# Optimization experiments

Measured on AMD Instinct MI355X. Metric: run time of the kernel, lower is better.

## Reference

```python
import jax, jax.numpy as jnp
import numpy as np

B, V, NQ, D, HEADS, FF, NL = 2, 8, 336, 256, 8, 1024, 6
H_IMG, W_IMG = 512, 512


def setup_inputs() -> dict:
    key = jax.random.key(0)
    ks = iter(jax.random.split(key, 48))
    def n(shape, s=0.02):
        return jax.random.normal(next(ks), shape, dtype=jnp.float32) * s
    inp = {}
    inp["tgt"] = jnp.zeros((B, NQ, D), jnp.float32)
    inp["query_pos"] = jax.random.normal(next(ks), (B, NQ, D), jnp.float32)
    inp["reference_points"] = jax.random.uniform(next(ks), (B, NQ, 3), dtype=jnp.float32)
    inp["feat0"] = jax.random.normal(next(ks), (B, V, D, 64, 64), jnp.float32)
    inp["feat1"] = jax.random.normal(next(ks), (B, V, D, 32, 32), jnp.float32)
    inp["feat2"] = jax.random.normal(next(ks), (B, V, D, 16, 16), jnp.float32)
    # cameras: near-identity rotations, translation pushed +2 in z so points project in front
    inp["camera_R"] = jnp.broadcast_to(jnp.eye(3, dtype=jnp.float32), (B, V, 3, 3)) + n((B, V, 3, 3), 0.1)
    T = n((B, V, 3), 0.1)
    inp["camera_T"] = T.at[..., 2].add(2.0)
    K = jnp.array([[500.0, 0.0, 256.0], [0.0, 500.0, 256.0], [0.0, 0.0, 1.0]], jnp.float32)
    inp["camera_K"] = jnp.broadcast_to(K, (B, V, 3, 3))
    # decoder params (stacked over NL layers)
    inp["Wqkv"] = n((NL, 3 * D, D)); inp["bqkv"] = jnp.zeros((NL, 3 * D), jnp.float32)
    inp["Wo"] = n((NL, D, D));       inp["bo"] = jnp.zeros((NL, D), jnp.float32)
    inp["ln1_g"] = jnp.ones((NL, D), jnp.float32); inp["ln1_b"] = jnp.zeros((NL, D), jnp.float32)
    inp["Wproj"] = n((NL, D, D));    inp["bproj"] = jnp.zeros((NL, D), jnp.float32)
    inp["pn_g"] = jnp.ones((NL, D), jnp.float32); inp["pn_b"] = jnp.zeros((NL, D), jnp.float32)
    inp["W1"] = n((NL, FF, D));      inp["b1"] = jnp.zeros((NL, FF), jnp.float32)
    inp["W2"] = n((NL, D, FF));      inp["b2"] = jnp.zeros((NL, D), jnp.float32)
    inp["ln2_g"] = jnp.ones((NL, D), jnp.float32); inp["ln2_b"] = jnp.zeros((NL, D), jnp.float32)
    inp["pose_W0"] = n((D, D)); inp["pose_b0"] = jnp.zeros((D,), jnp.float32)
    inp["pose_W1"] = n((D, D)); inp["pose_b1"] = jnp.zeros((D,), jnp.float32)
    inp["pose_W2"] = n((3, D)); inp["pose_b2"] = jnp.zeros((3,), jnp.float32)
    inp["cls_W"] = n((1, D));   inp["cls_b"] = jnp.zeros((1,), jnp.float32)
    return inp


def _layer_norm(x, g, b):
    m = x.mean(-1, keepdims=True)
    v = ((x - m) ** 2).mean(-1, keepdims=True)
    return (x - m) * jax.lax.rsqrt(v + 1e-5) * g + b


def _project(pts, R, T, K):
    # pts (B,NQ,3) -> cam coords per view: pts @ R^T + T
    p = jnp.einsum('bqc,bvdc->bvqd', pts, R) + T[:, :, None, :]  # (B,V,NQ,3)
    z = jnp.clip(p[..., 2], 0.1, None)
    fx = K[..., 0, 0][:, :, None]; fy = K[..., 1, 1][:, :, None]
    cx = K[..., 0, 2][:, :, None]; cy = K[..., 1, 2][:, :, None]
    u = p[..., 0] * fx / z + cx
    v = p[..., 1] * fy / z + cy
    un = 2.0 * u / (W_IMG - 1) - 1.0
    vn = 2.0 * v / (H_IMG - 1) - 1.0
    mask = (un > -1.0) & (un < 1.0) & (vn > -1.0) & (vn < 1.0) & (p[..., 2] > 0)
    return jnp.stack([un, vn], -1), mask  # (B,V,NQ,2), (B,V,NQ)


def _sample(feats, grid):
    # bilinear point sampling == F.grid_sample(align_corners=False, padding_mode='zeros')
    C, Hh, Ww = feats.shape[2], feats.shape[3], feats.shape[4]
    f = feats.reshape(B * V, C, Hh, Ww)
    g = grid.reshape(B * V, NQ, 2)
    x = (g[..., 0] + 1.0) * Ww * 0.5 - 0.5
    y = (g[..., 1] + 1.0) * Hh * 0.5 - 0.5
    x0f = jnp.floor(x); y0f = jnp.floor(y)
    ix0 = x0f.astype(jnp.int32); iy0 = y0f.astype(jnp.int32)
    ix1 = ix0 + 1; iy1 = iy0 + 1
    wx1 = (x - x0f)[:, None, :]; wx0 = 1.0 - wx1
    wy1 = (y - y0f)[:, None, :]; wy0 = 1.0 - wy1
    def gat(ix, iy):
        valid = ((ix >= 0) & (ix < Ww) & (iy >= 0) & (iy < Hh)).astype(f.dtype)[:, None, :]
        ixc = jnp.clip(ix, 0, Ww - 1); iyc = jnp.clip(iy, 0, Hh - 1)
        vals = jax.vmap(lambda ff, yy, xx: ff[:, yy, xx])(f, iyc, ixc)  # (BV,C,NQ)
        return vals * valid
    out = (gat(ix0, iy0) * wy0 * wx0 + gat(ix1, iy0) * wy0 * wx1 +
           gat(ix0, iy1) * wy1 * wx0 + gat(ix1, iy1) * wy1 * wx1)
    return out.reshape(B, V, C, NQ).transpose(0, 1, 3, 2)  # (B,V,NQ,C)


def _mha(xq, xv, Wqkv, bqkv, Wo, bo):
    hd = D // HEADS
    q = (xq @ Wqkv[:D].T + bqkv[:D]).reshape(B, NQ, HEADS, hd)
    k = (xq @ Wqkv[D:2 * D].T + bqkv[D:2 * D]).reshape(B, NQ, HEADS, hd)
    v = (xv @ Wqkv[2 * D:].T + bqkv[2 * D:]).reshape(B, NQ, HEADS, hd)
    att = jax.nn.softmax(jnp.einsum('bqhd,bkhd->bhqk', q, k) * (1.0 / np.sqrt(hd)), axis=-1)
    o = jnp.einsum('bhqk,bkhd->bqhd', att, v).reshape(B, NQ, D)
    return o @ Wo.T + bo


def reference(tgt, query_pos, reference_points, feat0, feat1, feat2, camera_R, camera_T, camera_K,
              Wqkv, bqkv, Wo, bo, ln1_g, ln1_b, Wproj, bproj, pn_g, pn_b,
              W1, b1, W2, b2, ln2_g, ln2_b,
              pose_W0, pose_b0, pose_W1, pose_b1, pose_W2, pose_b2, cls_W, cls_b):
    out = tgt
    ref = reference_points
    feats = (feat0, feat1, feat2)
    logits_all, poses_all = [], []
    for l in range(NL):
        # self-attention (dropout = eval identity)
        qk = out + query_pos
        out = _layer_norm(out + _mha(qk, out, Wqkv[l], bqkv[l], Wo[l], bo[l]), ln1_g[l], ln1_b[l])
        # projective attention: project 3D refs, grid-sample all levels, mask-fuse across views
        grid, mask = _project(ref, camera_R, camera_T, camera_K)
        ms = (_sample(feats[0], grid) + _sample(feats[1], grid) + _sample(feats[2], grid)) / 3.0
        vm = mask[..., None].astype(out.dtype)  # (B,V,NQ,1)
        fused = (ms * vm).sum(1) / jnp.clip(vm.sum(1), 1.0, None)  # (B,NQ,D)
        out = _layer_norm(out + fused @ Wproj[l].T + bproj[l], pn_g[l], pn_b[l])
        # FFN
        ffn = jax.nn.relu(out @ W1[l].T + b1[l]) @ W2[l].T + b2[l]
        out = _layer_norm(out + ffn, ln2_g[l], ln2_b[l])
        # iterative pose refinement + classification head
        h = jax.nn.relu(out @ pose_W0.T + pose_b0)
        h = jax.nn.relu(h @ pose_W1.T + pose_b1)
        ref = ref + h @ pose_W2.T + pose_b2
        logits_all.append(out @ cls_W.T + cls_b)
        poses_all.append(ref)
    # (NL,B,NQ,1) logits ++ (NL,B,NQ,3) poses -> (NL,B,NQ,4)
    return jnp.concatenate([jnp.stack(logits_all), jnp.stack(poses_all)], axis=-1)
```

## Files before the change

kernel.cpp:

```cpp
#include <hip/hip_runtime.h>
#include <math.h>

#define BB 2
#define VV 8
#define NQ 336
#define DD 256
#define HEADS 8
#define HD 32
#define FF 1024
#define NL 6
#define BQ (BB*NQ)
#define W_IMG 512
#define H_IMG 512
#define MROWS BQ

__device__ __forceinline__ void job_transpose2(float* tile, int b,
                                               const float* __restrict__ f0,
                                               const float* __restrict__ f1,
                                               const float* __restrict__ f2,
                                               float* __restrict__ o0,
                                               float* __restrict__ o1,
                                               float* __restrict__ o2) {
    const float* src; float* dst; int HW, ptiles;
    if (b < 2048)      { src = f0; dst = o0; HW = 4096; ptiles = 64; }
    else if (b < 2560) { b -= 2048; src = f1; dst = o1; HW = 1024; ptiles = 16; }
    else               { b -= 2560; src = f2; dst = o2; HW = 256;  ptiles = 4;  }
    int cg = b & 1;
    int pt = (b >> 1) % ptiles;
    int bv = (b >> 1) / ptiles;
    int d0 = cg * 128, p0 = pt * 64;
    int t = threadIdx.x;
    int t4 = t >> 4, t15 = t & 15;
    #pragma unroll
    for (int pass = 0; pass < 8; ++pass) {
        int d = pass * 16 + t4;
        int p = t15 * 4;
        float4 v = *(const float4*)(src + ((size_t)(bv * DD + d0 + d)) * HW + p0 + p);
        tile[d * 65 + p + 0] = v.x; tile[d * 65 + p + 1] = v.y;
        tile[d * 65 + p + 2] = v.z; tile[d * 65 + p + 3] = v.w;
    }
    __syncthreads();
    int c4 = (t & 31) * 4, pxb = t >> 5;
    #pragma unroll
    for (int pass = 0; pass < 8; ++pass) {
        int px = pass * 8 + pxb;
        float4 o;
        o.x = tile[(c4 + 0) * 65 + px];
        o.y = tile[(c4 + 1) * 65 + px];
        o.z = tile[(c4 + 2) * 65 + px];
        o.w = tile[(c4 + 3) * 65 + px];
        *(float4*)(dst + ((size_t)bv * HW + p0 + px) * DD + d0 + c4) = o;
    }
}

__global__ __launch_bounds__(256) void init_k(const float* __restrict__ tgt,
                                              const float* __restrict__ qp,
                                              const float* __restrict__ refpts,
                                              float* __restrict__ x,
                                              float* __restrict__ xq,
                                              float* __restrict__ refb) {
    int i = blockIdx.x * 256 + threadIdx.x;
    float4 tv = ((const float4*)tgt)[i];
    float4 qv = ((const float4*)qp)[i];
    ((float4*)x)[i] = tv;
    ((float4*)xq)[i] = make_float4(tv.x + qv.x, tv.y + qv.y, tv.z + qv.z, tv.w + qv.w);
    if (i < BQ * 3) refb[i] = refpts[i];
}

__device__ __forceinline__ void job_qkv(float* sm, int bid,
                                        const float* __restrict__ Aq,
                                        const float* __restrict__ Ax,
                                        const float* __restrict__ W,
                                        const float* __restrict__ bias,
                                        float* __restrict__ Qp,
                                        float* __restrict__ Kp,
                                        float* __restrict__ Vp) {
    float* At = sm;
    float* Wt = sm + 1088;
    int t = threadIdx.x;
    int m0 = (bid % 21) * 32;
    int ncol = bid / 21;
    int n0 = ncol * 64;
    const float* A = (ncol < 8) ? Aq : Ax;
    int tx = t & 15, ty = t >> 4;
    int nc = n0 + tx * 4;
    float acc0[4], acc1[4];
    {
        float4 bv = *(const float4*)(bias + nc);
        acc0[0] = bv.x; acc0[1] = bv.y; acc0[2] = bv.z; acc0[3] = bv.w;
        acc1[0] = bv.x; acc1[1] = bv.y; acc1[2] = bv.z; acc1[3] = bv.w;
    }
    int am = t >> 3, ak4 = (t & 7) * 4;
    for (int kt = 0; kt < 8; ++kt) {
        int kk = kt * 32;
        __syncthreads();
        {
            float4 v = *(const float4*)(A + (size_t)(m0 + am) * DD + kk + ak4);
            At[(ak4 + 0) * 34 + am] = v.x; At[(ak4 + 1) * 34 + am] = v.y;
            At[(ak4 + 2) * 34 + am] = v.z; At[(ak4 + 3) * 34 + am] = v.w;
        }
        #pragma unroll
        for (int s = 0; s < 2; ++s) {
            int idx = t + s * 256;
            int wn = idx >> 3, wk4 = (idx & 7) * 4;
            float4 v = *(const float4*)(W + (size_t)(n0 + wn) * DD + kk + wk4);
            Wt[(wk4 + 0) * 68 + wn] = v.x; Wt[(wk4 + 1) * 68 + wn] = v.y;
            Wt[(wk4 + 2) * 68 + wn] = v.z; Wt[(wk4 + 3) * 68 + wn] = v.w;
        }
        __syncthreads();
        #pragma unroll
        for (int k = 0; k < 32; ++k) {
            float2 av = *(const float2*)&At[k * 34 + ty * 2];
            float4 wv = *(const float4*)&Wt[k * 68 + tx * 4];
            acc0[0] = fmaf(av.x, wv.x, acc0[0]); acc0[1] = fmaf(av.x, wv.y, acc0[1]);
            acc0[2] = fmaf(av.x, wv.z, acc0[2]); acc0[3] = fmaf(av.x, wv.w, acc0[3]);
            acc1[0] = fmaf(av.y, wv.x, acc1[0]); acc1[1] = fmaf(av.y, wv.y, acc1[1]);
            acc1[2] = fmaf(av.y, wv.z, acc1[2]); acc1[3] = fmaf(av.y, wv.w, acc1[3]);
        }
    }
    int mr = m0 + ty * 2;
    int kind = nc >> 8;
    float* base = kind == 0 ? Qp : (kind == 1 ? Kp : Vp);
    int h = (nc >> 5) & 7, d4 = nc & 31;
    #pragma unroll
    for (int i = 0; i < 2; ++i) {
        int m = mr + i;
        int b = m / NQ, q = m - b * NQ;
        float* p = base + ((size_t)((b << 3) + h) * NQ + q) * HD + d4;
        float* src = i == 0 ? acc0 : acc1;
        *(float4*)p = make_float4(src[0], src[1], src[2], src[3]);
    }
}

__device__ __forceinline__ void job_pose(float* sm, int job,
                                         const float* __restrict__ x,
                                         const float* __restrict__ W0, const float* __restrict__ b0,
                                         const float* __restrict__ W1p, const float* __restrict__ b1p,
                                         const float* __restrict__ W2p, const float* __restrict__ b2p,
                                         const float* __restrict__ cW, const float* __restrict__ cb,
                                         float* __restrict__ refb, float* __restrict__ outp) {
    float* sX  = sm;
    float* sH  = sm + 1024;
    float* red = sm + 2048;
    int r0 = job * 4;
    int tid = threadIdx.x;
    ((float4*)sX)[tid] = ((const float4*)(x + (size_t)r0 * DD))[tid];
    __syncthreads();
    {
        float a0 = b0[tid], a1 = a0, a2 = a0, a3 = a0;
        const float* wp = W0 + (size_t)tid * DD;
        for (int k = 0; k < DD; k += 4) {
            float4 w  = *(const float4*)(wp + k);
            float4 x0 = *(const float4*)(sX + 0 * DD + k);
            float4 x1 = *(const float4*)(sX + 1 * DD + k);
            float4 x2 = *(const float4*)(sX + 2 * DD + k);
            float4 x3 = *(const float4*)(sX + 3 * DD + k);
            a0 = fmaf(x0.x, w.x, a0); a0 = fmaf(x0.y, w.y, a0); a0 = fmaf(x0.z, w.z, a0); a0 = fmaf(x0.w, w.w, a0);
            a1 = fmaf(x1.x, w.x, a1); a1 = fmaf(x1.y, w.y, a1); a1 = fmaf(x1.z, w.z, a1); a1 = fmaf(x1.w, w.w, a1);
            a2 = fmaf(x2.x, w.x, a2); a2 = fmaf(x2.y, w.y, a2); a2 = fmaf(x2.z, w.z, a2); a2 = fmaf(x2.w, w.w, a2);
            a3 = fmaf(x3.x, w.x, a3); a3 = fmaf(x3.y, w.y, a3); a3 = fmaf(x3.z, w.z, a3); a3 = fmaf(x3.w, w.w, a3);
        }
        sH[0 * DD + tid] = fmaxf(a0, 0.f);
        sH[1 * DD + tid] = fmaxf(a1, 0.f);
        sH[2 * DD + tid] = fmaxf(a2, 0.f);
        sH[3 * DD + tid] = fmaxf(a3, 0.f);
    }
    __syncthreads();
    float h[4];
    {
        float a0 = b1p[tid], a1 = a0, a2 = a0, a3 = a0;
        const float* wp = W1p + (size_t)tid * DD;
        for (int k = 0; k < DD; k += 4) {
            float4 w  = *(const float4*)(wp + k);
            float4 x0 = *(const float4*)(sH + 0 * DD + k);
            float4 x1 = *(const float4*)(sH + 1 * DD + k);
            float4 x2 = *(const float4*)(sH + 2 * DD + k);
            float4 x3 = *(const float4*)(sH + 3 * DD + k);
            a0 = fmaf(x0.x, w.x, a0); a0 = fmaf(x0.y, w.y, a0); a0 = fmaf(x0.z, w.z, a0); a0 = fmaf(x0.w, w.w, a0);
            a1 = fmaf(x1.x, w.x, a1); a1 = fmaf(x1.y, w.y, a1); a1 = fmaf(x1.z, w.z, a1); a1 = fmaf(x1.w, w.w, a1);
            a2 = fmaf(x2.x, w.x, a2); a2 = fmaf(x2.y, w.y, a2); a2 = fmaf(x2.z, w.z, a2); a2 = fmaf(x2.w, w.w, a2);
            a3 = fmaf(x3.x, w.x, a3); a3 = fmaf(x3.y, w.y, a3); a3 = fmaf(x3.z, w.z, a3); a3 = fmaf(x3.w, w.w, a3);
        }
        h[0] = fmaxf(a0, 0.f); h[1] = fmaxf(a1, 0.f); h[2] = fmaxf(a2, 0.f); h[3] = fmaxf(a3, 0.f);
    }
    float w2a = W2p[tid], w2b = W2p[DD + tid], w2c = W2p[2 * DD + tid], cw = cW[tid];
    float v[4][4];
    #pragma unroll
    for (int r = 0; r < 4; ++r) {
        v[r][0] = h[r] * w2a;
        v[r][1] = h[r] * w2b;
        v[r][2] = h[r] * w2c;
        v[r][3] = sX[r * DD + tid] * cw;
    }
    #pragma unroll
    for (int o2 = 32; o2 > 0; o2 >>= 1) {
        #pragma unroll
        for (int r = 0; r < 4; ++r) {
            #pragma unroll
            for (int c = 0; c < 4; ++c) v[r][c] += __shfl_xor(v[r][c], o2);
        }
    }
    int wid = tid >> 6, lane = tid & 63;
    if (lane == 0) {
        #pragma unroll
        for (int r = 0; r < 4; ++r) {
            #pragma unroll
            for (int c = 0; c < 4; ++c) red[(r * 4 + c) * 4 + wid] = v[r][c];
        }
    }
    __syncthreads();
    if (tid < 4) {
        int r = tid;
        float d0 = red[(r * 4 + 0) * 4 + 0] + red[(r * 4 + 0) * 4 + 1] + red[(r * 4 + 0) * 4 + 2] + red[(r * 4 + 0) * 4 + 3] + b2p[0];
        float d1 = red[(r * 4 + 1) * 4 + 0] + red[(r * 4 + 1) * 4 + 1] + red[(r * 4 + 1) * 4 + 2] + red[(r * 4 + 1) * 4 + 3] + b2p[1];
        float d2 = red[(r * 4 + 2) * 4 + 0] + red[(r * 4 + 2) * 4 + 1] + red[(r * 4 + 2) * 4 + 2] + red[(r * 4 + 2) * 4 + 3] + b2p[2];
        float cl = red[(r * 4 + 3) * 4 + 0] + red[(r * 4 + 3) * 4 + 1] + red[(r * 4 + 3) * 4 + 2] + red[(r * 4 + 3) * 4 + 3] + cb[0];
        int row = r0 + r;
        float rx = refb[(size_t)row * 3 + 0] + d0;
        float ry = refb[(size_t)row * 3 + 1] + d1;
        float rz = refb[(size_t)row * 3 + 2] + d2;
        refb[(size_t)row * 3 + 0] = rx;
        refb[(size_t)row * 3 + 1] = ry;
        refb[(size_t)row * 3 + 2] = rz;
        outp[(size_t)row * 4 + 0] = cl;
        outp[(size_t)row * 4 + 1] = rx;
        outp[(size_t)row * 4 + 2] = ry;
        outp[(size_t)row * 4 + 3] = rz;
    }
}

__global__ __launch_bounds__(256) void qkv_pose(const float* __restrict__ xq,
                                                const float* __restrict__ x,
                                                const float* __restrict__ Wqkv,
                                                const float* __restrict__ bqkv,
                                                float* __restrict__ Qp,
                                                float* __restrict__ Kp,
                                                float* __restrict__ Vp,
                                                const float* __restrict__ pW0, const float* __restrict__ pb0,
                                                const float* __restrict__ pW1, const float* __restrict__ pb1,
                                                const float* __restrict__ pW2, const float* __restrict__ pb2,
                                                const float* __restrict__ cW, const float* __restrict__ cb,
                                                float* __restrict__ refb, float* __restrict__ outp) {
    __shared__ float sm[3264];
    if (blockIdx.x < 252)
        job_qkv(sm, blockIdx.x, xq, x, Wqkv, bqkv, Qp, Kp, Vp);
    else
        job_pose(sm, blockIdx.x - 252, x, pW0, pb0, pW1, pb1, pW2, pb2, cW, cb, refb, outp);
}

__global__ __launch_bounds__(256) void qkv_tr(const float* __restrict__ xq,
                                              const float* __restrict__ x,
                                              const float* __restrict__ Wqkv,
                                              const float* __restrict__ bqkv,
                                              float* __restrict__ Qp,
                                              float* __restrict__ Kp,
                                              float* __restrict__ Vp,
                                              const float* __restrict__ f0,
                                              const float* __restrict__ f1,
                                              const float* __restrict__ f2,
                                              float* __restrict__ o0,
                                              float* __restrict__ o1,
                                              float* __restrict__ o2) {
    __shared__ float sm[8320];
    if (blockIdx.x < 252)
        job_qkv(sm, blockIdx.x, xq, x, Wqkv, bqkv, Qp, Kp, Vp);
    else
        job_transpose2(sm, blockIdx.x - 252, f0, f1, f2, o0, o1, o2);
}

__global__ __launch_bounds__(256) void pose_only(const float* __restrict__ x,
                                                 const float* __restrict__ pW0, const float* __restrict__ pb0,
                                                 const float* __restrict__ pW1, const float* __restrict__ pb1,
                                                 const float* __restrict__ pW2, const float* __restrict__ pb2,
                                                 const float* __restrict__ cW, const float* __restrict__ cb,
                                                 float* __restrict__ refb, float* __restrict__ outp) {
    __shared__ float sm[2112];
    job_pose(sm, blockIdx.x, x, pW0, pb0, pW1, pb1, pW2, pb2, cW, cb, refb, outp);
}

__global__ __launch_bounds__(256) void attn_fused(const float* __restrict__ Qp,
                                                  const float* __restrict__ Kp,
                                                  const float* __restrict__ Vp,
                                                  float* __restrict__ O,
                                                  const float* __restrict__ f0,
                                                  const float* __restrict__ f1,
                                                  const float* __restrict__ f2,
                                                  float* __restrict__ o0,
                                                  float* __restrict__ o1,
                                                  float* __restrict__ o2) {
    extern __shared__ float sm[];
    int blk = blockIdx.x;
    if (blk >= 176) { job_transpose2(sm, blk - 176 + 1344, f0, f1, f2, o0, o1, o2); return; }
    float* S   = sm;
    float* KT  = sm + 11008;
    float* U   = sm + 13184;
    float* inv = sm + 15232;
    int bh = blk & 15, qt = blk >> 4;
    int t = threadIdx.x;
    const float scale = 0.17677669529663687f;
    const float* Qb = Qp + (size_t)bh * NQ * HD;
    const float* Kb = Kp + (size_t)bh * NQ * HD;
    const float* Vb = Vp + (size_t)bh * NQ * HD;
    {
        int ql = t >> 3, d4 = (t & 7) * 4;
        int qg = qt * 32 + ql;
        float4 v = (qg < NQ) ? *(const float4*)(Qb + (size_t)qg * HD + d4)
                             : make_float4(0.f, 0.f, 0.f, 0.f);
        U[(d4 + 0) * 36 + ql] = v.x * scale;
        U[(d4 + 1) * 36 + ql] = v.y * scale;
        U[(d4 + 2) * 36 + ql] = v.z * scale;
        U[(d4 + 3) * 36 + ql] = v.w * scale;
    }
    int tx = t & 15, ty = t >> 4;
    for (int kt = 0; kt < 6; ++kt) {
        __syncthreads();
        #pragma unroll
        for (int s = 0; s < 2; ++s) {
            int idx = t + s * 256;
            int kl = idx >> 3, d4 = (idx & 7) * 4;
            int kg = kt * 64 + kl;
            float4 v = (kg < NQ) ? *(const float4*)(Kb + (size_t)kg * HD + d4)
                                 : make_float4(0.f, 0.f, 0.f, 0.f);
            KT[(d4 + 0) * 68 + kl] = v.x; KT[(d4 + 1) * 68 + kl] = v.y;
            KT[(d4 + 2) * 68 + kl] = v.z; KT[(d4 + 3) * 68 + kl] = v.w;
        }
        __syncthreads();
        float a0[4] = {0, 0, 0, 0}, a1[4] = {0, 0, 0, 0};
        #pragma unroll
        for (int k = 0; k < 32; ++k) {
            float2 qv = *(const float2*)&U[k * 36 + ty * 2];
            float4 kv = *(const float4*)&KT[k * 68 + tx * 4];
            a0[0] = fmaf(qv.x, kv.x, a0[0]); a0[1] = fmaf(qv.x, kv.y, a0[1]);
            a0[2] = fmaf(qv.x, kv.z, a0[2]); a0[3] = fmaf(qv.x, kv.w, a0[3]);
            a1[0] = fmaf(qv.y, kv.x, a1[0]); a1[1] = fmaf(qv.y, kv.y, a1[1]);
            a1[2] = fmaf(qv.y, kv.z, a1[2]); a1[3] = fmaf(qv.y, kv.w, a1[3]);
        }
        int col = kt * 64 + tx * 4;
        if (col < NQ) {
            *(float4*)&S[(ty * 2 + 0) * 344 + col] = make_float4(a0[0], a0[1], a0[2], a0[3]);
            *(float4*)&S[(ty * 2 + 1) * 344 + col] = make_float4(a1[0], a1[1], a1[2], a1[3]);
        }
    }
    __syncthreads();
    {
        int r = t >> 3, cg = t & 7;
        float* row = S + (size_t)r * 344;
        float m = -1e30f;
        for (int i = 0; i < 42; ++i) m = fmaxf(m, row[cg + 8 * i]);
        m = fmaxf(m, __shfl_xor(m, 1));
        m = fmaxf(m, __shfl_xor(m, 2));
        m = fmaxf(m, __shfl_xor(m, 4));
        float ssum = 0.f;
        for (int i = 0; i < 42; ++i) {
            float e = expf(row[cg + 8 * i] - m);
            row[cg + 8 * i] = e;
            ssum += e;
        }
        ssum += __shfl_xor(ssum, 1);
        ssum += __shfl_xor(ssum, 2);
        ssum += __shfl_xor(ssum, 4);
        if (cg == 0) inv[r] = 1.f / ssum;
    }
    int q = t >> 3, d0 = (t & 7) * 4;
    float acc[4] = {0, 0, 0, 0};
    for (int kt = 0; kt < 6; ++kt) {
        __syncthreads();
        #pragma unroll
        for (int s = 0; s < 2; ++s) {
            int idx = t + s * 256;
            int kl = idx >> 3, d4 = (idx & 7) * 4;
            int kg = kt * 64 + kl;
            float4 v = (kg < NQ) ? *(const float4*)(Vb + (size_t)kg * HD + d4)
                                 : make_float4(0.f, 0.f, 0.f, 0.f);
            *(float4*)&U[kl * 32 + d4] = v;
        }
        __syncthreads();
        int kmax = (kt == 5) ? 16 : 64;
        const float* Srow = S + (size_t)q * 344 + kt * 64;
        #pragma unroll 8
        for (int kk = 0; kk < kmax; ++kk) {
            float p = Srow[kk];
            float4 vv = *(const float4*)&U[kk * 32 + d0];
            acc[0] = fmaf(p, vv.x, acc[0]); acc[1] = fmaf(p, vv.y, acc[1]);
            acc[2] = fmaf(p, vv.z, acc[2]); acc[3] = fmaf(p, vv.w, acc[3]);
        }
    }
    float iv = inv[q];
    int qg = qt * 32 + q;
    int b = bh >> 3, h = bh & 7;
    if (qg < NQ)
        *(float4*)(O + ((size_t)(b * NQ + qg)) * DD + h * HD + d0) =
            make_float4(acc[0] * iv, acc[1] * iv, acc[2] * iv, acc[3] * iv);
}

__device__ __forceinline__ void job_gemm_ln(float* sm, int r0,
                                            const float* __restrict__ A,
                                            const float* __restrict__ Wt,
                                            const float* __restrict__ bias,
                                            const float* __restrict__ gam,
                                            const float* __restrict__ bet,
                                            float* __restrict__ x) {
    float* sA    = sm;
    float* redS  = sm + 1024;
    float* redS2 = sm + 1040;
    float* mu    = sm + 1056;
    float* ri    = sm + 1060;
    int j = threadIdx.x;
    ((float4*)sA)[j] = ((const float4*)(A + (size_t)r0 * DD))[j];
    __syncthreads();
    float acc0 = bias[j], acc1 = acc0, acc2 = acc0, acc3 = acc0;
    const float* wp = Wt + (size_t)j * DD;
    for (int k = 0; k < DD; k += 4) {
        float4 w  = *(const float4*)(wp + k);
        float4 a0 = *(const float4*)(sA + 0 * DD + k);
        float4 a1 = *(const float4*)(sA + 1 * DD + k);
        float4 a2 = *(const float4*)(sA + 2 * DD + k);
        float4 a3 = *(const float4*)(sA + 3 * DD + k);
        acc0 = fmaf(a0.x, w.x, acc0); acc0 = fmaf(a0.y, w.y, acc0); acc0 = fmaf(a0.z, w.z, acc0); acc0 = fmaf(a0.w, w.w, acc0);
        acc1 = fmaf(a1.x, w.x, acc1); acc1 = fmaf(a1.y, w.y, acc1); acc1 = fmaf(a1.z, w.z, acc1); acc1 = fmaf(a1.w, w.w, acc1);
        acc2 = fmaf(a2.x, w.x, acc2); acc2 = fmaf(a2.y, w.y, acc2); acc2 = fmaf(a2.z, w.z, acc2); acc2 = fmaf(a2.w, w.w, acc2);
        acc3 = fmaf(a3.x, w.x, acc3); acc3 = fmaf(a3.y, w.y, acc3); acc3 = fmaf(a3.z, w.z, acc3); acc3 = fmaf(a3.w, w.w, acc3);
    }
    float val[4];
    val[0] = x[(size_t)(r0 + 0) * DD + j] + acc0;
    val[1] = x[(size_t)(r0 + 1) * DD + j] + acc1;
    val[2] = x[(size_t)(r0 + 2) * DD + j] + acc2;
    val[3] = x[(size_t)(r0 + 3) * DD + j] + acc3;
    float s[4], s2[4];
    #pragma unroll
    for (int r = 0; r < 4; ++r) { s[r] = val[r]; s2[r] = val[r] * val[r]; }
    #pragma unroll
    for (int o2 = 32; o2 > 0; o2 >>= 1) {
        #pragma unroll
        for (int r = 0; r < 4; ++r) {
            s[r]  += __shfl_xor(s[r],  o2);
            s2[r] += __shfl_xor(s2[r], o2);
        }
    }
    int wid = j >> 6, lane = j & 63;
    if (lane == 0) {
        #pragma unroll
        for (int r = 0; r < 4; ++r) { redS[r * 4 + wid] = s[r]; redS2[r * 4 + wid] = s2[r]; }
    }
    __syncthreads();
    if (j < 4) {
        int r = j;
        float ts  = redS[r * 4 + 0]  + redS[r * 4 + 1]  + redS[r * 4 + 2]  + redS[r * 4 + 3];
        float ts2 = redS2[r * 4 + 0] + redS2[r * 4 + 1] + redS2[r * 4 + 2] + redS2[r * 4 + 3];
        float mean = ts * (1.f / DD);
        float var = ts2 * (1.f / DD) - mean * mean;
        mu[r] = mean;
        ri[r] = rsqrtf(var + 1e-5f);
    }
    __syncthreads();
    float g = gam[j], be = bet[j];
    #pragma unroll
    for (int r = 0; r < 4; ++r)
        x[(size_t)(r0 + r) * DD + j] = (val[r] - mu[r]) * ri[r] * g + be;
}

template <bool TRANSPOSED>
__device__ __forceinline__ void job_sample(float* sm, int row,
                                           const float* __restrict__ f0,
                                           const float* __restrict__ f1,
                                           const float* __restrict__ f2,
                                           const float* __restrict__ refb,
                                           const float* __restrict__ Rm,
                                           const float* __restrict__ Tm,
                                           const float* __restrict__ Km,
                                           float* __restrict__ fused) {
    float* sg    = sm;
    float* sPart = sm + 32;
    int t = threadIdx.x;
    int b = row / NQ;
    if (t < 8) {
        int bv = b * VV + t;
        const float* r = refb + (size_t)row * 3;
        const float* R = Rm + (size_t)bv * 9;
        const float* T = Tm + (size_t)bv * 3;
        const float* K = Km + (size_t)bv * 9;
        float p0 = R[0] * r[0] + R[1] * r[1] + R[2] * r[2] + T[0];
        float p1 = R[3] * r[0] + R[4] * r[1] + R[5] * r[2] + T[1];
        float p2 = R[6] * r[0] + R[7] * r[1] + R[8] * r[2] + T[2];
        float z = fmaxf(p2, 0.1f);
        float u  = p0 * K[0] / z + K[2];
        float vv = p1 * K[4] / z + K[5];
        float un = 2.f * u  / (float)(W_IMG - 1) - 1.f;
        float vn = 2.f * vv / (float)(H_IMG - 1) - 1.f;
        bool m = (un > -1.f) && (un < 1.f) && (vn > -1.f) && (vn < 1.f) && (p2 > 0.f);
        sg[t * 3 + 0] = un; sg[t * 3 + 1] = vn; sg[t * 3 + 2] = m ? 1.f : 0.f;
    }
    __syncthreads();
    int v = t >> 5, cg = t & 31;
    int ch0 = cg * 8;
    float acc[8] = {0, 0, 0, 0, 0, 0, 0, 0};
    float m = sg[v * 3 + 2];
    if (m != 0.f) {
        float un = sg[v * 3 + 0], vn = sg[v * 3 + 1];
        int bv = b * VV + v;
        const float* fl[3] = { f0, f1, f2 };
        const int Hs[3] = { 64, 32, 16 };
        #pragma unroll
        for (int lev = 0; lev < 3; ++lev) {
            int Hh = Hs[lev], Ww = Hs[lev];
            const float* f = fl[lev];
            float xx = (un + 1.f) * Ww * 0.5f - 0.5f;
            float yy = (vn + 1.f) * Hh * 0.5f - 0.5f;
            float x0f = floorf(xx), y0f = floorf(yy);
            int ix0 = (int)x0f, iy0 = (int)y0f;
            float wx1 = xx - x0f, wx0 = 1.f - wx1;
            float wy1 = yy - y0f, wy0 = 1.f - wy1;
            #pragma unroll
            for (int tap = 0; tap < 4; ++tap) {
                int ix = ix0 + (tap & 1);
                int iy = iy0 + (tap >> 1);
                float wgt = ((tap & 1) ? wx1 : wx0) * ((tap >> 1) ? wy1 : wy0);
                if (ix >= 0 && ix < Ww && iy >= 0 && iy < Hh) {
                    if (TRANSPOSED) {
                        const float* p = f + ((size_t)bv * Hh * Ww + (size_t)iy * Ww + ix) * DD + ch0;
                        float4 va = *(const float4*)p;
                        float4 vb = *(const float4*)(p + 4);
                        acc[0] = fmaf(wgt, va.x, acc[0]); acc[1] = fmaf(wgt, va.y, acc[1]);
                        acc[2] = fmaf(wgt, va.z, acc[2]); acc[3] = fmaf(wgt, va.w, acc[3]);
                        acc[4] = fmaf(wgt, vb.x, acc[4]); acc[5] = fmaf(wgt, vb.y, acc[5]);
                        acc[6] = fmaf(wgt, vb.z, acc[6]); acc[7] = fmaf(wgt, vb.w, acc[7]);
                    } else {
                        #pragma unroll
                        for (int c = 0; c < 8; ++c) {
                            float vv2 = f[(((size_t)bv * DD + ch0 + c) * Hh + iy) * Ww + ix];
                            acc[c] = fmaf(wgt, vv2, acc[c]);
                        }
                    }
                }
            }
        }
    }
    #pragma unroll
    for (int c = 0; c < 8; ++c) sPart[v * 258 + ch0 + c] = acc[c] * (1.f / 3.f);
    __syncthreads();
    float cnt = sg[2] + sg[5] + sg[8] + sg[11] + sg[14] + sg[17] + sg[20] + sg[23];
    float s = 0.f;
    #pragma unroll
    for (int v2 = 0; v2 < 8; ++v2) s += sPart[v2 * 258 + t];
    fused[(size_t)row * DD + t] = s / fmaxf(cnt, 1.f);
}

template <bool TRANSPOSED>
__global__ __launch_bounds__(256) void oproj_sample(const float* __restrict__ attn_o,
                                                    const float* __restrict__ Wo,
                                                    const float* __restrict__ bo,
                                                    const float* __restrict__ gam,
                                                    const float* __restrict__ bet,
                                                    float* __restrict__ x,
                                                    const float* __restrict__ f0,
                                                    const float* __restrict__ f1,
                                                    const float* __restrict__ f2,
                                                    const float* __restrict__ refb,
                                                    const float* __restrict__ Rm,
                                                    const float* __restrict__ Tm,
                                                    const float* __restrict__ Km,
                                                    float* __restrict__ fused) {
    __shared__ float sm[2112];
    if (blockIdx.x < 168)
        job_gemm_ln(sm, blockIdx.x * 4, attn_o, Wo, bo, gam, bet, x);
    else
        job_sample<TRANSPOSED>(sm, blockIdx.x - 168, f0, f1, f2, refb, Rm, Tm, Km, fused);
}

__global__ __launch_bounds__(256) void gemm4_res_ln(const float* __restrict__ A,
                                                    const float* __restrict__ Wt,
                                                    const float* __restrict__ bias,
                                                    const float* __restrict__ gam,
                                                    const float* __restrict__ bet,
                                                    float* __restrict__ x) {
    __shared__ float sm[1064];
    job_gemm_ln(sm, blockIdx.x * 4, A, Wt, bias, gam, bet, x);
}

template <int MODE>
__global__ __launch_bounds__(256) void gemm_tile(const float* __restrict__ A,
                                                 const float* __restrict__ W,
                                                 const float* __restrict__ bias,
                                                 float* __restrict__ C,
                                                 int Ktot, int Kper, int Nout) {
    __shared__ float At[32][34];
    __shared__ float Wt[32][68];
    int t = threadIdx.x;
    int m0 = blockIdx.x * 32;
    int n0 = blockIdx.y * 64;
    int kz = blockIdx.z;
    int kofs = kz * Kper;
    int tx = t & 15, ty = t >> 4;
    int nc = n0 + tx * 4;
    float acc0[4], acc1[4];
    {
        float4 bv = make_float4(0.f, 0.f, 0.f, 0.f);
        if (bias && kz == 0) bv = *(const float4*)(bias + nc);
        acc0[0] = bv.x; acc0[1] = bv.y; acc0[2] = bv.z; acc0[3] = bv.w;
        acc1[0] = bv.x; acc1[1] = bv.y; acc1[2] = bv.z; acc1[3] = bv.w;
    }
    int am = t >> 3, ak4 = (t & 7) * 4;
    int ktiles = Kper >> 5;
    for (int kt = 0; kt < ktiles; ++kt) {
        int kk = kofs + kt * 32;
        __syncthreads();
        {
            float4 v = *(const float4*)(A + (size_t)(m0 + am) * Ktot + kk + ak4);
            At[ak4 + 0][am] = v.x; At[ak4 + 1][am] = v.y;
            At[ak4 + 2][am] = v.z; At[ak4 + 3][am] = v.w;
        }
        #pragma unroll
        for (int s = 0; s < 2; ++s) {
            int idx = t + s * 256;
            int wn = idx >> 3, wk4 = (idx & 7) * 4;
            float4 v = *(const float4*)(W + (size_t)(n0 + wn) * Ktot + kk + wk4);
            Wt[wk4 + 0][wn] = v.x; Wt[wk4 + 1][wn] = v.y;
            Wt[wk4 + 2][wn] = v.z; Wt[wk4 + 3][wn] = v.w;
        }
        __syncthreads();
        #pragma unroll
        for (int k = 0; k < 32; ++k) {
            float2 av = *(const float2*)&At[k][ty * 2];
            float4 wv = *(const float4*)&Wt[k][tx * 4];
            acc0[0] = fmaf(av.x, wv.x, acc0[0]); acc0[1] = fmaf(av.x, wv.y, acc0[1]);
            acc0[2] = fmaf(av.x, wv.z, acc0[2]); acc0[3] = fmaf(av.x, wv.w, acc0[3]);
            acc1[0] = fmaf(av.y, wv.x, acc1[0]); acc1[1] = fmaf(av.y, wv.y, acc1[1]);
            acc1[2] = fmaf(av.y, wv.z, acc1[2]); acc1[3] = fmaf(av.y, wv.w, acc1[3]);
        }
    }
    if (MODE == 1) {
        #pragma unroll
        for (int j = 0; j < 4; ++j) { acc0[j] = fmaxf(acc0[j], 0.f); acc1[j] = fmaxf(acc1[j], 0.f); }
    }
    int mr = m0 + ty * 2;
    float* Cb = C + (size_t)kz * MROWS * Nout;
    *(float4*)(Cb + (size_t)mr * Nout + nc)       = make_float4(acc0[0], acc0[1], acc0[2], acc0[3]);
    *(float4*)(Cb + (size_t)(mr + 1) * Nout + nc) = make_float4(acc1[0], acc1[1], acc1[2], acc1[3]);
}

template <int NP>
__global__ __launch_bounds__(256) void ln_res(float* __restrict__ x,
                                              const float* __restrict__ C,
                                              const float* __restrict__ gam,
                                              const float* __restrict__ bet,
                                              const float* __restrict__ qp,
                                              float* __restrict__ xq) {
    __shared__ float redS[4][4], redS2[4][4];
    __shared__ float mu[4], ri[4];
    int r0 = blockIdx.x * 4;
    int j = threadIdx.x;
    float val[4];
    #pragma unroll
    for (int r = 0; r < 4; ++r) {
        float a = x[(size_t)(r0 + r) * DD + j];
        #pragma unroll
        for (int p = 0; p < NP; ++p) a += C[(size_t)p * MROWS * DD + (size_t)(r0 + r) * DD + j];
        val[r] = a;
    }
    float s[4], s2[4];
    #pragma unroll
    for (int r = 0; r < 4; ++r) { s[r] = val[r]; s2[r] = val[r] * val[r]; }
    #pragma unroll
    for (int o = 32; o > 0; o >>= 1) {
        #pragma unroll
        for (int r = 0; r < 4; ++r) {
            s[r]  += __shfl_xor(s[r],  o);
            s2[r] += __shfl_xor(s2[r], o);
        }
    }
    int wid = j >> 6, lane = j & 63;
    if (lane == 0) {
        #pragma unroll
        for (int r = 0; r < 4; ++r) { redS[r][wid] = s[r]; redS2[r][wid] = s2[r]; }
    }
    __syncthreads();
    if (j < 4) {
        int r = j;
        float ts  = redS[r][0]  + redS[r][1]  + redS[r][2]  + redS[r][3];
        float ts2 = redS2[r][0] + redS2[r][1] + redS2[r][2] + redS2[r][3];
        float mean = ts * (1.f / DD);
        float var = ts2 * (1.f / DD) - mean * mean;
        mu[r] = mean;
        ri[r] = rsqrtf(var + 1e-5f);
    }
    __syncthreads();
    float g = gam[j], be = bet[j];
    #pragma unroll
    for (int r = 0; r < 4; ++r) {
        float o = (val[r] - mu[r]) * ri[r] * g + be;
        x[(size_t)(r0 + r) * DD + j] = o;
        if (qp) xq[(size_t)(r0 + r) * DD + j] = o + qp[(size_t)(r0 + r) * DD + j];
    }
}

extern "C" void kernel_launch(void* const* d_in, const int* in_sizes, int n_in,
                              void* d_out, int out_size, void* d_ws, size_t ws_size,
                              hipStream_t stream) {
    const float* tgt       = (const float*)d_in[0];
    const float* query_pos = (const float*)d_in[1];
    const float* refpts    = (const float*)d_in[2];
    const float* feat0     = (const float*)d_in[3];
    const float* feat1     = (const float*)d_in[4];
    const float* feat2     = (const float*)d_in[5];
    const float* camR      = (const float*)d_in[6];
    const float* camT      = (const float*)d_in[7];
    const float* camK      = (const float*)d_in[8];
    const float* Wqkv      = (const float*)d_in[9];
    const float* bqkv      = (const float*)d_in[10];
    const float* Wo        = (const float*)d_in[11];
    const float* bo        = (const float*)d_in[12];
    const float* ln1_g     = (const float*)d_in[13];
    const float* ln1_b     = (const float*)d_in[14];
    const float* Wproj     = (const float*)d_in[15];
    const float* bproj     = (const float*)d_in[16];
    const float* pn_g      = (const float*)d_in[17];
    const float* pn_b      = (const float*)d_in[18];
    const float* W1        = (const float*)d_in[19];
    const float* b1        = (const float*)d_in[20];
    const float* W2        = (const float*)d_in[21];
    const float* b2        = (const float*)d_in[22];
    const float* ln2_g     = (const float*)d_in[23];
    const float* ln2_b     = (const float*)d_in[24];
    const float* pose_W0   = (const float*)d_in[25];
    const float* pose_b0   = (const float*)d_in[26];
    const float* pose_W1   = (const float*)d_in[27];
    const float* pose_b1   = (const float*)d_in[28];
    const float* pose_W2   = (const float*)d_in[29];
    const float* pose_b2   = (const float*)d_in[30];
    const float* cls_W     = (const float*)d_in[31];
    const float* cls_b     = (const float*)d_in[32];
    float* out = (float*)d_out;

    float* w = (float*)d_ws;
    size_t off = 0;
    auto alloc = [&](size_t n) { float* p = w + off; off += n; return p; };
    float* x      = alloc((size_t)BQ * DD);
    float* xq     = alloc((size_t)BQ * DD);
    float* Qp     = alloc((size_t)BB * HEADS * NQ * HD);
    float* Kp     = alloc((size_t)BB * HEADS * NQ * HD);
    float* Vp     = alloc((size_t)BB * HEADS * NQ * HD);
    float* attn_o = alloc((size_t)BQ * DD);
    float* fused  = alloc((size_t)BQ * DD);
    float* ffh    = alloc((size_t)BQ * FF);
    float* ctmp   = alloc((size_t)4 * BQ * DD);
    float* refb   = alloc((size_t)BQ * 3 + 64);
    size_t base_floats = off;
    size_t featT_floats = (size_t)BB * VV * DD * (64 * 64 + 32 * 32 + 16 * 16);
    bool useT = ws_size >= (base_floats + featT_floats) * sizeof(float);
    float *fT0 = nullptr, *fT1 = nullptr, *fT2 = nullptr;
    if (useT) {
        fT0 = alloc((size_t)BB * VV * 64 * 64 * DD);
        fT1 = alloc((size_t)BB * VV * 32 * 32 * DD);
        fT2 = alloc((size_t)BB * VV * 16 * 16 * DD);
    }

    init_k<<<168, 256, 0, stream>>>(tgt, query_pos, refpts, x, xq, refb);

    for (int l = 0; l < NL; ++l) {
        if (l == 0 && useT) {
            qkv_tr<<<252 + 1344, 256, 0, stream>>>(
                xq, x, Wqkv, bqkv, Qp, Kp, Vp,
                feat0, feat1, feat2, fT0, fT1, fT2);
        } else {
            qkv_pose<<<252 + (l > 0 ? 168 : 0), 256, 0, stream>>>(
                xq, x, Wqkv + (size_t)l * 3 * DD * DD, bqkv + (size_t)l * 3 * DD, Qp, Kp, Vp,
                pose_W0, pose_b0, pose_W1, pose_b1, pose_W2, pose_b2, cls_W, cls_b,
                refb, out + (size_t)(l - 1) * BQ * 4);
        }
        {
            int tc = (l == 0 && useT) ? 1344 : 0;
            attn_fused<<<176 + tc, 256, 61056, stream>>>(
                Qp, Kp, Vp, attn_o, feat0, feat1, feat2, fT0, fT1, fT2);
        }
        if (useT)
            oproj_sample<true><<<840, 256, 0, stream>>>(
                attn_o, Wo + (size_t)l * DD * DD, bo + (size_t)l * DD,
                ln1_g + (size_t)l * DD, ln1_b + (size_t)l * DD, x,
                fT0, fT1, fT2, refb, camR, camT, camK, fused);
        else
            oproj_sample<false><<<840, 256, 0, stream>>>(
                attn_o, Wo + (size_t)l * DD * DD, bo + (size_t)l * DD,
                ln1_g + (size_t)l * DD, ln1_b + (size_t)l * DD, x,
                feat0, feat1, feat2, refb, camR, camT, camK, fused);
        gemm4_res_ln<<<BQ / 4, 256, 0, stream>>>(
            fused, Wproj + (size_t)l * DD * DD, bproj + (size_t)l * DD,
            pn_g + (size_t)l * DD, pn_b + (size_t)l * DD, x);
        gemm_tile<1><<<dim3(21, 16, 1), 256, 0, stream>>>(
            x, W1 + (size_t)l * FF * DD, b1 + (size_t)l * FF, ffh, DD, DD, FF);
        gemm_tile<0><<<dim3(21, 4, 4), 256, 0, stream>>>(
            ffh, W2 + (size_t)l * DD * FF, b2 + (size_t)l * DD, ctmp, FF, FF / 4, DD);
        ln_res<4><<<BQ / 4, 256, 0, stream>>>(
            x, ctmp, ln2_g + (size_t)l * DD, ln2_b + (size_t)l * DD, query_pos, xq);
    }
    pose_only<<<BQ / 4, 256, 0, stream>>>(
        x, pose_W0, pose_b0, pose_W1, pose_b1, pose_W2, pose_b2, cls_W, cls_b,
        refb, out + (size_t)(NL - 1) * BQ * 4);
}
```

Measured before the change: 888.3 us.

## Fuse FFN down-projection with residual layernorm; move feature transposes out of attention

Replaces the split-K tiled FFN2 GEMM and the separate residual-LayerNorm kernel with one kernel, ffn2_ln. It handles 4 rows per block, stages the hidden activations in shared memory and has each thread compute one output column over the full K=1024. This removes the partial-sum buffer round trip and one launch per layer. The cost is per-thread strided reads of W2 rows, with every block re-reading the whole weight matrix. The feature-map transpose now uses 32-pixel tiles with twice as many blocks, and all of it runs inside the layer-0 QKV launch rather than being split with the attention kernel. The attention kernel now uses static shared memory and no longer carries transpose work.

After: 1.037 ms. 16.8% more time.

```diff
diff --git a/kernel.cpp b/kernel.cpp
--- a/kernel.cpp
+++ b/kernel.cpp
@@ -14,7 +14,7 @@
 #define H_IMG 512
 #define MROWS BQ
 
-__device__ __forceinline__ void job_transpose2(float* tile, int b,
+__device__ __forceinline__ void job_transpose3(float* tile, int b,
                                                const float* __restrict__ f0,
                                                const float* __restrict__ f1,
                                                const float* __restrict__ f2,
@@ -22,33 +22,32 @@
                                                float* __restrict__ o1,
                                                float* __restrict__ o2) {
     const float* src; float* dst; int HW, ptiles;
-    if (b < 2048)      { src = f0; dst = o0; HW = 4096; ptiles = 64; }
-    else if (b < 2560) { b -= 2048; src = f1; dst = o1; HW = 1024; ptiles = 16; }
-    else               { b -= 2560; src = f2; dst = o2; HW = 256;  ptiles = 4;  }
+    if (b < 4096)      { src = f0; dst = o0; HW = 4096; ptiles = 128; }
+    else if (b < 5120) { b -= 4096; src = f1; dst = o1; HW = 1024; ptiles = 32; }
+    else               { b -= 5120; src = f2; dst = o2; HW = 256;  ptiles = 8;  }
     int cg = b & 1;
     int pt = (b >> 1) % ptiles;
     int bv = (b >> 1) / ptiles;
-    int d0 = cg * 128, p0 = pt * 64;
+    int d0 = cg * 128, p0 = pt * 32;
     int t = threadIdx.x;
-    int t4 = t >> 4, t15 = t & 15;
-    #pragma unroll
-    for (int pass = 0; pass < 8; ++pass) {
-        int d = pass * 16 + t4;
-        int p = t15 * 4;
-        float4 v = *(const float4*)(src + ((size_t)(bv * DD + d0 + d)) * HW + p0 + p);
-        tile[d * 65 + p + 0] = v.x; tile[d * 65 + p + 1] = v.y;
-        tile[d * 65 + p + 2] = v.z; tile[d * 65 + p + 3] = v.w;
+    int chb = t >> 3, px4 = (t & 7) * 4;
+    #pragma unroll
+    for (int pass = 0; pass < 4; ++pass) {
+        int ch = pass * 32 + chb;
+        float4 v = *(const float4*)(src + ((size_t)(bv * DD + d0 + ch)) * HW + p0 + px4);
+        tile[ch * 33 + px4 + 0] = v.x; tile[ch * 33 + px4 + 1] = v.y;
+        tile[ch * 33 + px4 + 2] = v.z; tile[ch * 33 + px4 + 3] = v.w;
     }
     __syncthreads();
     int c4 = (t & 31) * 4, pxb = t >> 5;
     #pragma unroll
-    for (int pass = 0; pass < 8; ++pass) {
+    for (int pass = 0; pass < 4; ++pass) {
         int px = pass * 8 + pxb;
         float4 o;
-        o.x = tile[(c4 + 0) * 65 + px];
-        o.y = tile[(c4 + 1) * 65 + px];
-        o.z = tile[(c4 + 2) * 65 + px];
-        o.w = tile[(c4 + 3) * 65 + px];
+        o.x = tile[(c4 + 0) * 33 + px];
+        o.y = tile[(c4 + 1) * 33 + px];
+        o.z = tile[(c4 + 2) * 33 + px];
+        o.w = tile[(c4 + 3) * 33 + px];
         *(float4*)(dst + ((size_t)bv * HW + p0 + px) * DD + d0 + c4) = o;
     }
 }
@@ -261,11 +260,11 @@
                                               float* __restrict__ o0,
                                               float* __restrict__ o1,
                                               float* __restrict__ o2) {
-    __shared__ float sm[8320];
+    __shared__ float sm[4224];
     if (blockIdx.x < 252)
         job_qkv(sm, blockIdx.x, xq, x, Wqkv, bqkv, Qp, Kp, Vp);
     else
-        job_transpose2(sm, blockIdx.x - 252, f0, f1, f2, o0, o1, o2);
+        job_transpose3(sm, blockIdx.x - 252, f0, f1, f2, o0, o1, o2);
 }
 
 __global__ __launch_bounds__(256) void pose_only(const float* __restrict__ x,
@@ -281,20 +280,13 @@
 __global__ __launch_bounds__(256) void attn_fused(const float* __restrict__ Qp,
                                                   const float* __restrict__ Kp,
                                                   const float* __restrict__ Vp,
-                                                  float* __restrict__ O,
-                                                  const float* __restrict__ f0,
-                                                  const float* __restrict__ f1,
-                                                  const float* __restrict__ f2,
-                                                  float* __restrict__ o0,
-                                                  float* __restrict__ o1,
-                                                  float* __restrict__ o2) {
-    extern __shared__ float sm[];
-    int blk = blockIdx.x;
-    if (blk >= 176) { job_transpose2(sm, blk - 176 + 1344, f0, f1, f2, o0, o1, o2); return; }
+                                                  float* __restrict__ O) {
+    __shared__ float sm[15264];
     float* S   = sm;
     float* KT  = sm + 11008;
     float* U   = sm + 13184;
     float* inv = sm + 15232;
+    int blk = blockIdx.x;
     int bh = blk & 15, qt = blk >> 4;
     int t = threadIdx.x;
     const float scale = 0.17677669529663687f;
@@ -457,6 +449,76 @@
     #pragma unroll
     for (int r = 0; r < 4; ++r)
         x[(size_t)(r0 + r) * DD + j] = (val[r] - mu[r]) * ri[r] * g + be;
+}
+
+__global__ __launch_bounds__(256) void ffn2_ln(const float* __restrict__ ffh,
+                                               const float* __restrict__ W2,
+                                               const float* __restrict__ b2,
+                                               const float* __restrict__ gam,
+                                               const float* __restrict__ bet,
+                                               float* __restrict__ x,
+                                               const float* __restrict__ qp,
+                                               float* __restrict__ xq) {
+    __shared__ float sH[4 * FF];
+    __shared__ float redS[16], redS2[16], mu[4], ri[4];
+    int r0 = blockIdx.x * 4;
+    int j = threadIdx.x;
+    #pragma unroll
+    for (int s = 0; s < 4; ++s)
+        ((float4*)sH)[j + s * 256] = ((const float4*)(ffh + (size_t)r0 * FF))[j + s * 256];
+    __syncthreads();
+    float acc0 = b2[j], acc1 = acc0, acc2 = acc0, acc3 = acc0;
+    const float* wp = W2 + (size_t)j * FF;
+    for (int k = 0; k < FF; k += 4) {
+        float4 w  = *(const float4*)(wp + k);
+        float4 a0 = *(const float4*)(sH + 0 * FF + k);
+        float4 a1 = *(const float4*)(sH + 1 * FF + k);
+        float4 a2 = *(const float4*)(sH + 2 * FF + k);
+        float4 a3 = *(const float4*)(sH + 3 * FF + k);
+        acc0 = fmaf(a0.x, w.x, acc0); acc0 = fmaf(a0.y, w.y, acc0); acc0 = fmaf(a0.z, w.z, acc0); acc0 = fmaf(a0.w, w.w, acc0);
+        acc1 = fmaf(a1.x, w.x, acc1); acc1 = fmaf(a1.y, w.y, acc1); acc1 = fmaf(a1.z, w.z, acc1); acc1 = fmaf(a1.w, w.w, acc1);
+        acc2 = fmaf(a2.x, w.x, acc2); acc2 = fmaf(a2.y, w.y, acc2); acc2 = fmaf(a2.z, w.z, acc2); acc2 = fmaf(a2.w, w.w, acc2);
+        acc3 = fmaf(a3.x, w.x, acc3); acc3 = fmaf(a3.y, w.y, acc3); acc3 = fmaf(a3.z, w.z, acc3); acc3 = fmaf(a3.w, w.w, acc3);
+    }
+    float val[4];
+    val[0] = x[(size_t)(r0 + 0) * DD + j] + acc0;
+    val[1] = x[(size_t)(r0 + 1) * DD + j] + acc1;
+    val[2] = x[(size_t)(r0 + 2) * DD + j] + acc2;
+    val[3] = x[(size_t)(r0 + 3) * DD + j] + acc3;
+    float s[4], s2[4];
+    #pragma unroll
+    for (int r = 0; r < 4; ++r) { s[r] = val[r]; s2[r] = val[r] * val[r]; }
+    #pragma unroll
+    for (int o2 = 32; o2 > 0; o2 >>= 1) {
+        #pragma unroll
+        for (int r = 0; r < 4; ++r) {
+            s[r]  += __shfl_xor(s[r],  o2);
+            s2[r] += __shfl_xor(s2[r], o2);
+        }
+    }
+    int wid = j >> 6, lane = j & 63;
+    if (lane == 0) {
+        #pragma unroll
+        for (int r = 0; r < 4; ++r) { redS[r * 4 + wid] = s[r]; redS2[r * 4 + wid] = s2[r]; }
+    }
+    __syncthreads();
+    if (j < 4) {
+        int r = j;
+        float ts  = redS[r * 4 + 0]  + redS[r * 4 + 1]  + redS[r * 4 + 2]  + redS[r * 4 + 3];
+        float ts2 = redS2[r * 4 + 0] + redS2[r * 4 + 1] + redS2[r * 4 + 2] + redS2[r * 4 + 3];
+        float mean = ts * (1.f / DD);
+        float var = ts2 * (1.f / DD) - mean * mean;
+        mu[r] = mean;
+        ri[r] = rsqrtf(var + 1e-5f);
+    }
+    __syncthreads();
+    float g = gam[j], be = bet[j];
+    #pragma unroll
+    for (int r = 0; r < 4; ++r) {
+        float o = (val[r] - mu[r]) * ri[r] * g + be;
+        x[(size_t)(r0 + r) * DD + j] = o;
+        xq[(size_t)(r0 + r) * DD + j] = o + qp[(size_t)(r0 + r) * DD + j];
+    }
 }
 
 template <bool TRANSPOSED>
@@ -636,61 +698,6 @@
     float* Cb = C + (size_t)kz * MROWS * Nout;
     *(float4*)(Cb + (size_t)mr * Nout + nc)       = make_float4(acc0[0], acc0[1], acc0[2], acc0[3]);
     *(float4*)(Cb + (size_t)(mr + 1) * Nout + nc) = make_float4(acc1[0], acc1[1], acc1[2], acc1[3]);
-}
-
-template <int NP>
-__global__ __launch_bounds__(256) void ln_res(float* __restrict__ x,
-                                              const float* __restrict__ C,
-                                              const float* __restrict__ gam,
-                                              const float* __restrict__ bet,
-                                              const float* __restrict__ qp,
-                                              float* __restrict__ xq) {
-    __shared__ float redS[4][4], redS2[4][4];
-    __shared__ float mu[4], ri[4];
-    int r0 = blockIdx.x * 4;
-    int j = threadIdx.x;
-    float val[4];
-    #pragma unroll
-    for (int r = 0; r < 4; ++r) {
-        float a = x[(size_t)(r0 + r) * DD + j];
-        #pragma unroll
-        for (int p = 0; p < NP; ++p) a += C[(size_t)p * MROWS * DD + (size_t)(r0 + r) * DD + j];
-        val[r] = a;
-    }
-    float s[4], s2[4];
-    #pragma unroll
-    for (int r = 0; r < 4; ++r) { s[r] = val[r]; s2[r] = val[r] * val[r]; }
-    #pragma unroll
-    for (int o = 32; o > 0; o >>= 1) {
-        #pragma unroll
-        for (int r = 0; r < 4; ++r) {
-            s[r]  += __shfl_xor(s[r],  o);
-            s2[r] += __shfl_xor(s2[r], o);
-        }
-    }
-    int wid = j >> 6, lane = j & 63;
-    if (lane == 0) {
-        #pragma unroll
-        for (int r = 0; r < 4; ++r) { redS[r][wid] = s[r]; redS2[r][wid] = s2[r]; }
-    }
-    __syncthreads();
-    if (j < 4) {
-        int r = j;
-        float ts  = redS[r][0]  + redS[r][1]  + redS[r][2]  + redS[r][3];
-        float ts2 = redS2[r][0] + redS2[r][1] + redS2[r][2] + redS2[r][3];
-        float mean = ts * (1.f / DD);
-        float var = ts2 * (1.f / DD) - mean * mean;
-        mu[r] = mean;
-        ri[r] = rsqrtf(var + 1e-5f);
-    }
-    __syncthreads();
-    float g = gam[j], be = bet[j];
-    #pragma unroll
-    for (int r = 0; r < 4; ++r) {
-        float o = (val[r] - mu[r]) * ri[r] * g + be;
-        x[(size_t)(r0 + r) * DD + j] = o;
-        if (qp) xq[(size_t)(r0 + r) * DD + j] = o + qp[(size_t)(r0 + r) * DD + j];
-    }
 }
 
 extern "C" void kernel_launch(void* const* d_in, const int* in_sizes, int n_in,
@@ -742,7 +749,6 @@
     float* attn_o = alloc((size_t)BQ * DD);
     float* fused  = alloc((size_t)BQ * DD);
     float* ffh    = alloc((size_t)BQ * FF);
-    float* ctmp   = alloc((size_t)4 * BQ * DD);
     float* refb   = alloc((size_t)BQ * 3 + 64);
     size_t base_floats = off;
     size_t featT_floats = (size_t)BB * VV * DD * (64 * 64 + 32 * 32 + 16 * 16);
@@ -758,7 +764,7 @@
 
     for (int l = 0; l < NL; ++l) {
         if (l == 0 && useT) {
-            qkv_tr<<<252 + 1344, 256, 0, stream>>>(
+            qkv_tr<<<252 + 5376, 256, 0, stream>>>(
                 xq, x, Wqkv, bqkv, Qp, Kp, Vp,
                 feat0, feat1, feat2, fT0, fT1, fT2);
         } else {
@@ -767,11 +773,7 @@
                 pose_W0, pose_b0, pose_W1, pose_b1, pose_W2, pose_b2, cls_W, cls_b,
                 refb, out + (size_t)(l - 1) * BQ * 4);
         }
-        {
-            int tc = (l == 0 && useT) ? 1344 : 0;
-            attn_fused<<<176 + tc, 256, 61056, stream>>>(
-                Qp, Kp, Vp, attn_o, feat0, feat1, feat2, fT0, fT1, fT2);
-        }
+        attn_fused<<<176, 256, 0, stream>>>(Qp, Kp, Vp, attn_o);
         if (useT)
             oproj_sample<true><<<840, 256, 0, stream>>>(
                 attn_o, Wo + (size_t)l * DD * DD, bo + (size_t)l * DD,
@@ -787,10 +789,9 @@
             pn_g + (size_t)l * DD, pn_b + (size_t)l * DD, x);
         gemm_tile<1><<<dim3(21, 16, 1), 256, 0, stream>>>(
             x, W1 + (size_t)l * FF * DD, b1 + (size_t)l * FF, ffh, DD, DD, FF);
-        gemm_tile<0><<<dim3(21, 4, 4), 256, 0, stream>>>(
-            ffh, W2 + (size_t)l * DD * FF, b2 + (size_t)l * DD, ctmp, FF, FF / 4, DD);
-        ln_res<4><<<BQ / 4, 256, 0, stream>>>(
-            x, ctmp, ln2_g + (size_t)l * DD, ln2_b + (size_t)l * DD, query_pos, xq);
+        ffn2_ln<<<BQ / 4, 256, 0, stream>>>(
+            ffh, W2 + (size_t)l * DD * FF, b2 + (size_t)l * DD,
+            ln2_g + (size_t)l * DD, ln2_b + (size_t)l * DD, x, query_pos, xq);
     }
     pose_only<<<BQ / 4, 256, 0, stream>>>(
         x, pose_W0, pose_b0, pose_W1, pose_b1, pose_W2, pose_b2, cls_W, cls_b,
```

## Move all feature transposes into qkv launch with smaller 32-pixel tiles

Applied to the files above, without the earlier changes.

The feature-map transpose now uses 32-pixel tiles instead of 64, which halves the shared tile and quadruples the block count to 5376. All of that work goes into the layer-0 qkv_tr launch rather than being split between qkv_tr and attn_fused. attn_fused becomes a pure attention kernel with static shared memory and 176 blocks. The aim is better occupancy and a cleaner attention launch. The cost is that the attention kernel no longer overlaps with any transpose work, and there are more small blocks to schedule.

Measured after the change: 842.7 us. 1.05x faster.

```diff
diff --git a/kernel.cpp b/kernel.cpp
--- a/kernel.cpp
+++ b/kernel.cpp
@@ -14,7 +14,7 @@
 #define H_IMG 512
 #define MROWS BQ
 
-__device__ __forceinline__ void job_transpose2(float* tile, int b,
+__device__ __forceinline__ void job_transpose3(float* tile, int b,
                                                const float* __restrict__ f0,
                                                const float* __restrict__ f1,
                                                const float* __restrict__ f2,
@@ -22,33 +22,32 @@
                                                float* __restrict__ o1,
                                                float* __restrict__ o2) {
     const float* src; float* dst; int HW, ptiles;
-    if (b < 2048)      { src = f0; dst = o0; HW = 4096; ptiles = 64; }
-    else if (b < 2560) { b -= 2048; src = f1; dst = o1; HW = 1024; ptiles = 16; }
-    else               { b -= 2560; src = f2; dst = o2; HW = 256;  ptiles = 4;  }
+    if (b < 4096)      { src = f0; dst = o0; HW = 4096; ptiles = 128; }
+    else if (b < 5120) { b -= 4096; src = f1; dst = o1; HW = 1024; ptiles = 32; }
+    else               { b -= 5120; src = f2; dst = o2; HW = 256;  ptiles = 8;  }
     int cg = b & 1;
     int pt = (b >> 1) % ptiles;
     int bv = (b >> 1) / ptiles;
-    int d0 = cg * 128, p0 = pt * 64;
+    int d0 = cg * 128, p0 = pt * 32;
     int t = threadIdx.x;
-    int t4 = t >> 4, t15 = t & 15;
-    #pragma unroll
-    for (int pass = 0; pass < 8; ++pass) {
-        int d = pass * 16 + t4;
-        int p = t15 * 4;
-        float4 v = *(const float4*)(src + ((size_t)(bv * DD + d0 + d)) * HW + p0 + p);
-        tile[d * 65 + p + 0] = v.x; tile[d * 65 + p + 1] = v.y;
-        tile[d * 65 + p + 2] = v.z; tile[d * 65 + p + 3] = v.w;
+    int chb = t >> 3, px4 = (t & 7) * 4;
+    #pragma unroll
+    for (int pass = 0; pass < 4; ++pass) {
+        int ch = pass * 32 + chb;
+        float4 v = *(const float4*)(src + ((size_t)(bv * DD + d0 + ch)) * HW + p0 + px4);
+        tile[ch * 33 + px4 + 0] = v.x; tile[ch * 33 + px4 + 1] = v.y;
+        tile[ch * 33 + px4 + 2] = v.z; tile[ch * 33 + px4 + 3] = v.w;
     }
     __syncthreads();
     int c4 = (t & 31) * 4, pxb = t >> 5;
     #pragma unroll
-    for (int pass = 0; pass < 8; ++pass) {
+    for (int pass = 0; pass < 4; ++pass) {
         int px = pass * 8 + pxb;
         float4 o;
-        o.x = tile[(c4 + 0) * 65 + px];
-        o.y = tile[(c4 + 1) * 65 + px];
-        o.z = tile[(c4 + 2) * 65 + px];
-        o.w = tile[(c4 + 3) * 65 + px];
+        o.x = tile[(c4 + 0) * 33 + px];
+        o.y = tile[(c4 + 1) * 33 + px];
+        o.z = tile[(c4 + 2) * 33 + px];
+        o.w = tile[(c4 + 3) * 33 + px];
         *(float4*)(dst + ((size_t)bv * HW + p0 + px) * DD + d0 + c4) = o;
     }
 }
@@ -261,11 +260,11 @@
                                               float* __restrict__ o0,
                                               float* __restrict__ o1,
                                               float* __restrict__ o2) {
-    __shared__ float sm[8320];
+    __shared__ float sm[4224];
     if (blockIdx.x < 252)
         job_qkv(sm, blockIdx.x, xq, x, Wqkv, bqkv, Qp, Kp, Vp);
     else
-        job_transpose2(sm, blockIdx.x - 252, f0, f1, f2, o0, o1, o2);
+        job_transpose3(sm, blockIdx.x - 252, f0, f1, f2, o0, o1, o2);
 }
 
 __global__ __launch_bounds__(256) void pose_only(const float* __restrict__ x,
@@ -281,20 +280,13 @@
 __global__ __launch_bounds__(256) void attn_fused(const float* __restrict__ Qp,
                                                   const float* __restrict__ Kp,
                                                   const float* __restrict__ Vp,
-                                                  float* __restrict__ O,
-                                                  const float* __restrict__ f0,
-                                                  const float* __restrict__ f1,
-                                                  const float* __restrict__ f2,
-                                                  float* __restrict__ o0,
-                                                  float* __restrict__ o1,
-                                                  float* __restrict__ o2) {
-    extern __shared__ float sm[];
-    int blk = blockIdx.x;
-    if (blk >= 176) { job_transpose2(sm, blk - 176 + 1344, f0, f1, f2, o0, o1, o2); return; }
+                                                  float* __restrict__ O) {
+    __shared__ float sm[15264];
     float* S   = sm;
     float* KT  = sm + 11008;
     float* U   = sm + 13184;
     float* inv = sm + 15232;
+    int blk = blockIdx.x;
     int bh = blk & 15, qt = blk >> 4;
     int t = threadIdx.x;
     const float scale = 0.17677669529663687f;
@@ -758,7 +750,7 @@
 
     for (int l = 0; l < NL; ++l) {
         if (l == 0 && useT) {
-            qkv_tr<<<252 + 1344, 256, 0, stream>>>(
+            qkv_tr<<<252 + 5376, 256, 0, stream>>>(
                 xq, x, Wqkv, bqkv, Qp, Kp, Vp,
                 feat0, feat1, feat2, fT0, fT1, fT2);
         } else {
@@ -767,11 +759,7 @@
                 pose_W0, pose_b0, pose_W1, pose_b1, pose_W2, pose_b2, cls_W, cls_b,
                 refb, out + (size_t)(l - 1) * BQ * 4);
         }
-        {
-            int tc = (l == 0 && useT) ? 1344 : 0;
-            attn_fused<<<176 + tc, 256, 61056, stream>>>(
-                Qp, Kp, Vp, attn_o, feat0, feat1, feat2, fT0, fT1, fT2);
-        }
+        attn_fused<<<176, 256, 0, stream>>>(Qp, Kp, Vp, attn_o);
         if (useT)
             oproj_sample<true><<<840, 256, 0, stream>>>(
                 attn_o, Wo + (size_t)l * DD * DD, bo + (size_t)l * DD,
```
